# Kernel tuning notes

Measured on AMD Instinct MI355X. Metric: run time of the kernel, lower is better.

Reference implementation:

```python
import jax, jax.numpy as jnp
import numpy as np

T, B, I, H, LBL = 200, 1024, 128, 128, 4


def setup_inputs() -> dict:
    key = jax.random.key(0)
    ks = jax.random.split(key, 14)
    si = 1.0 / np.sqrt(I)
    sh = 1.0 / np.sqrt(H)
    inputs = jax.random.normal(ks[0], (T, B, I), jnp.float32)
    lengths = jnp.maximum(jax.random.randint(ks[1], (B,), 1, T + 1), LBL).astype(jnp.int32)
    return {
        "inputs": inputs,
        "lengths": lengths,
        "Wih_g": jax.random.normal(ks[2], (3 * H, I), jnp.float32) * si,
        "Whh_g": jax.random.normal(ks[3], (3 * H, H), jnp.float32) * sh,
        "bih_g": jax.random.normal(ks[4], (3 * H,), jnp.float32) * sh,
        "bhh_g": jax.random.normal(ks[5], (3 * H,), jnp.float32) * sh,
        "Wih_l": jax.random.normal(ks[6], (3 * H, I), jnp.float32) * si,
        "Whh_l": jax.random.normal(ks[7], (3 * H, H), jnp.float32) * sh,
        "bih_l": jax.random.normal(ks[8], (3 * H,), jnp.float32) * sh,
        "bhh_l": jax.random.normal(ks[9], (3 * H,), jnp.float32) * sh,
        "A1": jax.random.normal(ks[10], (H, H), jnp.float32) * sh,
        "A2": jax.random.normal(ks[11], (H, H), jnp.float32) * sh,
        "v1": jax.random.normal(ks[12], (1, H), jnp.float32) * sh,
        "label_len": LBL,
    }


def gru(x, Wih, Whh, bih, bhh):
    # x: [T, B, I] time-major. PyTorch GRU cell semantics.
    Bq, Hq = x.shape[1], Whh.shape[1]
    gi_all = jnp.einsum('tbi,gi->tbg', x, Wih) + bih  # precompute input projections [T,B,3H]
    def step(h, gi):
        gh = h @ Whh.T + bhh
        ir, iz, inn = jnp.split(gi, 3, axis=-1)
        hr, hz, hn = jnp.split(gh, 3, axis=-1)
        r = jax.nn.sigmoid(ir + hr)
        z = jax.nn.sigmoid(iz + hz)
        n = jnp.tanh(inn + r * hn)
        h = (1.0 - z) * n + z * h
        return h, h
    h0 = jnp.zeros((Bq, Hq), x.dtype)
    _, hs = jax.lax.scan(step, h0, gi_all)
    return hs  # [T, B, H]


def reference(inputs, lengths, Wih_g, Whh_g, bih_g, bhh_g,
              Wih_l, Whh_l, bih_l, bhh_l, A1, A2, v1, label_len):
    h_g = gru(inputs, Wih_g, Whh_g, bih_g, bhh_g)  # [T,B,H]
    h_l = gru(inputs, Wih_l, Whh_l, bih_l, bhh_l)  # [T,B,H]
    # attention score per step s: v1(sigmoid(A1 h_l + A2 h_g)), query-independent
    pre = jax.nn.sigmoid(jnp.einsum('tbh,gh->tbg', h_l, A1) +
                         jnp.einsum('tbh,gh->tbg', h_g, A2))
    scores = jnp.einsum('tbg,og->tbo', pre, v1)  # [T,B,1]
    # per-t output = cumsum_{s<=t}(score*h_l) + h_g[t]
    out = jnp.cumsum(scores * h_l, axis=0) + h_g  # [T,B,H]
    out_b = jnp.transpose(out, (1, 0, 2))  # [B,T,H]
    # gather last label_len timesteps of each sequence: h[b,k] = out[L_b-label_len+k, b]
    idx = lengths[:, None].astype(jnp.int32) - label_len + jnp.arange(label_len, dtype=jnp.int32)[None, :]
    idx = jnp.clip(idx, 0, out_b.shape[1] - 1)  # [B, label_len]
    h = jnp.take_along_axis(out_b, idx[:, :, None], axis=1)  # [B, label_len, H]
    return h
```

## Files before the change

### kernel.cpp

```cpp
#include <hip/hip_runtime.h>
#include <stdint.h>


typedef __attribute__((ext_vector_type(8))) short short8;
typedef __attribute__((ext_vector_type(4))) float float4v;

#define LDS_BARRIER() asm volatile("s_waitcnt lgkmcnt(0)\n\ts_barrier" ::: "memory")

__device__ inline float bf2f(unsigned short u){
  union { unsigned int i; float f; } v; v.i = ((unsigned int)u) << 16; return v.f;
}
__device__ inline unsigned short f2bf(float f){
  union { float f; unsigned int i; } v; v.f = f;
  unsigned int x = v.i;
  return (unsigned short)((x + 0x7fffu + ((x >> 16) & 1u)) >> 16);
}
__device__ inline float sigm(float x){ return __builtin_amdgcn_rcpf(1.0f + __expf(-x)); }

__global__ void k_prep(unsigned short* hl_slot, unsigned short* hg_slot, float* cum,
                       const float* A1, const float* A2, unsigned short* a12)
{
  int i = blockIdx.x * blockDim.x + threadIdx.x;
  hl_slot[i] = 0;
  hg_slot[i] = 0;
  cum[i] = 0.0f;
  if (i < 32768) {
    a12[i] = f2bf((i < 16384) ? A1[i] : A2[i - 16384]);
  }
}

__global__ void k_xcast(const float* __restrict__ x, unsigned short* __restrict__ xb)
{
  int i8 = blockIdx.x * blockDim.x + threadIdx.x;
  int t = i8 >> 14;
  int rem = i8 & 16383;
  int b = rem >> 4, c = rem & 15;
  int m = b & 15, bg = b >> 4;
  const float4* xf = (const float4*)(x + ((size_t)t * 131072 + (size_t)b * 128 + c * 8));
  float4 a = xf[0], bb = xf[1];
  short8 o;
  o[0]=(short)f2bf(a.x); o[1]=(short)f2bf(a.y); o[2]=(short)f2bf(a.z); o[3]=(short)f2bf(a.w);
  o[4]=(short)f2bf(bb.x); o[5]=(short)f2bf(bb.y); o[6]=(short)f2bf(bb.z); o[7]=(short)f2bf(bb.w);
  *(short8*)(xb + (size_t)t * 131072 + (size_t)bg * 2048 + c * 128 + m * 8) = o;
}

__global__ __launch_bounds__(512, 2) void k_scan(
    const unsigned short* __restrict__ xb,
    const float* __restrict__ Wih_g, const float* __restrict__ Whh_g,
    const float* __restrict__ bih_g, const float* __restrict__ bhh_g,
    const float* __restrict__ Wih_l, const float* __restrict__ Whh_l,
    const float* __restrict__ bih_l, const float* __restrict__ bhh_l,
    unsigned short* __restrict__ hl_seq, unsigned short* __restrict__ hg_seq,
    int tc, int t0)
{
  __shared__ __align__(16) unsigned short hb[2][2048];
  int tid = threadIdx.x;
  int w = tid >> 6, L = tid & 63, l15 = L & 15, q = L >> 4;
  int gru = blockIdx.x & 1;
  int bg = blockIdx.x >> 1;
  const float* Wih = gru ? Wih_l : Wih_g;
  const float* Whh = gru ? Whh_l : Whh_g;
  const float* bih = gru ? bih_l : bih_g;
  const float* bhh = gru ? bhh_l : bhh_g;
  unsigned short* myseq = gru ? hl_seq : hg_seq;

  int col = w * 16 + l15;
  int cch = w * 2 + (l15 >> 3);
  int cj  = l15 & 7;

  short8 Wi[3][4], Wh[3][4];
  #pragma unroll
  for (int G = 0; G < 3; G++) {
    int row = G * 128 + col;
    #pragma unroll
    for (int kf = 0; kf < 4; kf++) {
      const float4* p0 = (const float4*)(Wih + (size_t)row * 128 + kf * 32 + q * 8);
      const float4* p1 = (const float4*)(Whh + (size_t)row * 128 + kf * 32 + q * 8);
      float4 a0 = p0[0], a1 = p0[1], b0f = p1[0], b1f = p1[1];
      short8 si, sh;
      si[0]=(short)f2bf(a0.x); si[1]=(short)f2bf(a0.y); si[2]=(short)f2bf(a0.z); si[3]=(short)f2bf(a0.w);
      si[4]=(short)f2bf(a1.x); si[5]=(short)f2bf(a1.y); si[6]=(short)f2bf(a1.z); si[7]=(short)f2bf(a1.w);
      sh[0]=(short)f2bf(b0f.x); sh[1]=(short)f2bf(b0f.y); sh[2]=(short)f2bf(b0f.z); sh[3]=(short)f2bf(b0f.w);
      sh[4]=(short)f2bf(b1f.x); sh[5]=(short)f2bf(b1f.y); sh[6]=(short)f2bf(b1f.z); sh[7]=(short)f2bf(b1f.w);
      Wi[G][kf] = si; Wh[G][kf] = sh;
    }
  }
  float br  = bih[col]       + bhh[col];
  float bz  = bih[128 + col] + bhh[128 + col];
  float bin = bih[256 + col];
  float bnh = bhh[256 + col];

  float hold[4];
  #pragma unroll
  for (int r = 0; r < 4; r++) {
    int m = q * 4 + r;
    unsigned short u = myseq[(size_t)(tc - 1) * 131072 + (size_t)bg * 2048 + cch * 128 + m * 8 + cj];
    hold[r] = bf2f(u);
    hb[0][cch * 128 + m * 8 + cj] = u;
  }

  short8 x2[2][4];
  const unsigned short* xlane = xb + (size_t)bg * 2048 + q * 128 + l15 * 8;
  {
    const unsigned short* px = xlane + (size_t)t0 * 131072;
    #pragma unroll
    for (int kf = 0; kf < 4; kf++) x2[0][kf] = *(const short8*)(px + kf * 512);
    int t1 = t0 + (tc > 1 ? 1 : 0);
    const unsigned short* py = xlane + (size_t)t1 * 131072;
    #pragma unroll
    for (int kf = 0; kf < 4; kf++) x2[1][kf] = *(const short8*)(py + kf * 512);
  }
  __syncthreads();

  unsigned short* opq = myseq + (size_t)bg * 2048 + cch * 128 + q * 32 + cj;
  unsigned int* hbw = (unsigned int*)&hb[0][0];
  int wdw = (2 * w + (l15 >> 3)) * 64 + ((l15 & 6) >> 1);
  bool wlane = (L & 1) == 0;

  auto step = [&](int s, int pin, int pout) {
    short8 Ah[4];
    #pragma unroll
    for (int kf = 0; kf < 4; kf++)
      Ah[kf] = *(const short8*)&hb[pin][(kf * 4 + q) * 128 + l15 * 8];

    float4v rx = (float4v){0.f,0.f,0.f,0.f}, zx = rx, nx = rx;
    #pragma unroll
    for (int kf = 0; kf < 4; kf++) rx = __builtin_amdgcn_mfma_f32_16x16x32_bf16(x2[pin][kf], Wi[0][kf], rx, 0,0,0);
    #pragma unroll
    for (int kf = 0; kf < 4; kf++) zx = __builtin_amdgcn_mfma_f32_16x16x32_bf16(x2[pin][kf], Wi[1][kf], zx, 0,0,0);
    #pragma unroll
    for (int kf = 0; kf < 4; kf++) nx = __builtin_amdgcn_mfma_f32_16x16x32_bf16(x2[pin][kf], Wi[2][kf], nx, 0,0,0);

    {
      int t2 = t0 + (s + 2 < tc ? s + 2 : tc - 1);
      const unsigned short* px = xlane + (size_t)t2 * 131072;
      #pragma unroll
      for (int kf = 0; kf < 4; kf++) x2[pin][kf] = *(const short8*)(px + kf * 512);
    }

    float4v rh = (float4v){0.f,0.f,0.f,0.f}, zh = rh, nh = rh;
    #pragma unroll
    for (int kf = 0; kf < 4; kf++) rh = __builtin_amdgcn_mfma_f32_16x16x32_bf16(Ah[kf], Wh[0][kf], rh, 0,0,0);
    #pragma unroll
    for (int kf = 0; kf < 4; kf++) zh = __builtin_amdgcn_mfma_f32_16x16x32_bf16(Ah[kf], Wh[1][kf], zh, 0,0,0);
    #pragma unroll
    for (int kf = 0; kf < 4; kf++) nh = __builtin_amdgcn_mfma_f32_16x16x32_bf16(Ah[kf], Wh[2][kf], nh, 0,0,0);

    float cr[4], cz[4], cn[4];
    #pragma unroll
    for (int r = 0; r < 4; r++) { cr[r] = rx[r] + br; cz[r] = zx[r] + bz; cn[r] = nx[r] + bin; }

    unsigned int* hbo = hbw + pout * 1024 + wdw;
    #pragma unroll
    for (int r = 0; r < 4; r++) {
      float er = __expf(-(rh[r] + cr[r]));
      float ez = __expf(-(zh[r] + cz[r]));
      float pr = 1.0f + er, pz = 1.0f + ez;
      float inv = __builtin_amdgcn_rcpf(pr * pz);
      float rr = pz * inv;
      float zz = pr * inv;
      float y  = cn[r] + rr * (nh[r] + bnh);
      float em = __expf(-2.0f * y);
      float nn = 2.0f * __builtin_amdgcn_rcpf(1.0f + em) - 1.0f;
      float hn = nn + zz * (hold[r] - nn);
      hold[r] = hn;
      unsigned short hu = f2bf(hn);
      opq[r * 8] = hu;
      unsigned int hv = (unsigned int)hu;
      unsigned int ov = (unsigned int)__shfl_xor((int)hv, 1);
      if (wlane) hbo[(4 * q + r) * 4] = hv | (ov << 16);
    }
    opq += 131072;
    LDS_BARRIER();
  };

  int s = 0;
  for (; s + 1 < tc; s += 2) { step(s, 0, 1); step(s + 1, 1, 0); }
  if (s < tc) step(s, 0, 1);
}

__global__ __launch_bounds__(512) void k_score(const unsigned short* __restrict__ hl_seq,
                                               const unsigned short* __restrict__ hg_seq,
                                               const unsigned short* __restrict__ a12,
                                               const float* __restrict__ v1,
                                               float* __restrict__ score, int tc)
{
  __shared__ __align__(16) unsigned short M1[128][136];
  __shared__ __align__(16) unsigned short M2[128][136];
  int tid = threadIdx.x;
  int w = tid >> 6, L = tid & 63;
  int l15 = L & 15, q = L >> 4;
  int s = blockIdx.x;
  int bghalf = blockIdx.y * 32;

  #pragma unroll
  for (int it = 0; it < 4; it++) {
    int f8 = it * 512 + tid;
    *(short8*)&M1[f8 >> 4][(f8 & 15) * 8] = *(const short8*)(a12 + (size_t)f8 * 8);
    *(short8*)&M2[f8 >> 4][(f8 & 15) * 8] = *(const short8*)(a12 + 16384 + (size_t)f8 * 8);
  }
  __syncthreads();

  float v1v[8];
  #pragma unroll
  for (int nt = 0; nt < 8; nt++) v1v[nt] = v1[nt * 16 + l15];

  short8 Fl[4], Fg[4], Pl[4], Pg[4];
  {
    size_t base = (size_t)s * 131072 + (size_t)(bghalf + w) * 2048 + q * 128 + l15 * 8;
    #pragma unroll
    for (int kf = 0; kf < 4; kf++) {
      Fl[kf] = *(const short8*)(hl_seq + base + kf * 512);
      Fg[kf] = *(const short8*)(hg_seq + base + kf * 512);
    }
  }
  #pragma unroll
  for (int it = 0; it < 4; it++) {
    int bg = bghalf + it * 8 + w;
    if (it + 1 < 4) {
      size_t base = (size_t)s * 131072 + (size_t)(bghalf + (it + 1) * 8 + w) * 2048 + q * 128 + l15 * 8;
      #pragma unroll
      for (int kf = 0; kf < 4; kf++) {
        Pl[kf] = *(const short8*)(hl_seq + base + kf * 512);
        Pg[kf] = *(const short8*)(hg_seq + base + kf * 512);
      }
    }
    float4v acc[8];
    #pragma unroll
    for (int nt = 0; nt < 8; nt++) {
      float4v a = (float4v){0.f, 0.f, 0.f, 0.f};
      #pragma unroll
      for (int kf = 0; kf < 4; kf++)
        a = __builtin_amdgcn_mfma_f32_16x16x32_bf16(
            Fl[kf], *(const short8*)&M1[nt * 16 + l15][kf * 32 + q * 8], a, 0, 0, 0);
      #pragma unroll
      for (int kf = 0; kf < 4; kf++)
        a = __builtin_amdgcn_mfma_f32_16x16x32_bf16(
            Fg[kf], *(const short8*)&M2[nt * 16 + l15][kf * 32 + q * 8], a, 0, 0, 0);
      acc[nt] = a;
    }
    float p4[4];
    #pragma unroll
    for (int r = 0; r < 4; r++) {
      float sum = 0.f;
      #pragma unroll
      for (int nt = 0; nt < 8; nt++) sum += v1v[nt] * sigm(acc[nt][r]);
      sum += __shfl_xor(sum, 1, 16);
      sum += __shfl_xor(sum, 2, 16);
      sum += __shfl_xor(sum, 4, 16);
      sum += __shfl_xor(sum, 8, 16);
      p4[r] = sum;
    }
    if (l15 == 0) {
      #pragma unroll
      for (int r = 0; r < 4; r++)
        score[(size_t)(bg * 16 + q * 4 + r) * tc + s] = p4[r];
    }
    #pragma unroll
    for (int kf = 0; kf < 4; kf++) { Fl[kf] = Pl[kf]; Fg[kf] = Pg[kf]; }
  }
}

__global__ __launch_bounds__(256) void k_cum(const float* __restrict__ score,
                                             const unsigned short* __restrict__ hl_seq,
                                             const unsigned short* __restrict__ hg_seq,
                                             const int* __restrict__ lengths,
                                             float* __restrict__ cum,
                                             float* __restrict__ out, int tc, int t0)
{
  __shared__ __align__(16) unsigned short hlL[100 * 256];
  __shared__ float scL[2][100];
  int tid = threadIdx.x;
  int b2 = tid >> 7, j = tid & 127;
  int b0 = blockIdx.x * 2;
  int b = b0 + b2;
  int base = b2 * 128 + j;
  int bg0 = b0 >> 4, m0 = b0 & 15;

  float c = cum[(size_t)b * 128 + j];
  int cap0 = lengths[b] - 4;

  float hgv[4];
  #pragma unroll
  for (int d = 0; d < 4; d++) {
    int sl = cap0 + d - t0;
    hgv[d] = (sl >= 0 && sl < tc)
      ? bf2f(hg_seq[(size_t)sl * 131072 + (size_t)(b >> 4) * 2048 + (j >> 3) * 128 + (b & 15) * 8 + (j & 7)])
      : 0.f;
  }

  for (int seg = 0; seg < tc; seg += 100) {
    int len = (tc - seg < 100) ? (tc - seg) : 100;
    __syncthreads();
    for (int f8 = tid; f8 < len * 32; f8 += 256) {
      int sl = f8 >> 5, r8 = f8 & 31;
      int bb = r8 >> 4, ch = r8 & 15;
      *(short8*)&hlL[(size_t)f8 * 8] =
          *(const short8*)(hl_seq + (size_t)(seg + sl) * 131072 + (size_t)bg0 * 2048
                           + ch * 128 + (m0 + bb) * 8);
    }
    for (int i = tid; i < 2 * len; i += 256) {
      int bb = (i >= len) ? 1 : 0;
      int sl = i - bb * len;
      scL[bb][sl] = score[(size_t)(b0 + bb) * tc + seg + sl];
    }
    __syncthreads();

    int sl = 0;
    for (; sl + 5 <= len; sl += 5) {
      float h[5], sc[5];
      #pragma unroll
      for (int k = 0; k < 5; k++) {
        h[k] = bf2f(hlL[(size_t)(sl + k) * 256 + base]);
        sc[k] = scL[b2][sl + k];
      }
      #pragma unroll
      for (int k = 0; k < 5; k++) {
        c += sc[k] * h[k];
        int d = (t0 + seg + sl + k) - cap0;
        if ((unsigned)d < 4u)
          out[((size_t)b * 4 + d) * 128 + j] = c + hgv[d];
      }
    }
    for (; sl < len; sl++) {
      c += scL[b2][sl] * bf2f(hlL[(size_t)sl * 256 + base]);
      int d = (t0 + seg + sl) - cap0;
      if ((unsigned)d < 4u)
        out[((size_t)b * 4 + d) * 128 + j] = c + hgv[d];
    }
  }
  cum[(size_t)b * 128 + j] = c;
}

extern "C" void kernel_launch(void* const* d_in, const int* in_sizes, int n_in,
                              void* d_out, int out_size, void* d_ws, size_t ws_size,
                              hipStream_t stream)
{
  const float* x     = (const float*)d_in[0];
  const int* lengths = (const int*)d_in[1];
  const float* Wih_g = (const float*)d_in[2];
  const float* Whh_g = (const float*)d_in[3];
  const float* bih_g = (const float*)d_in[4];
  const float* bhh_g = (const float*)d_in[5];
  const float* Wih_l = (const float*)d_in[6];
  const float* Whh_l = (const float*)d_in[7];
  const float* bih_l = (const float*)d_in[8];
  const float* bhh_l = (const float*)d_in[9];
  const float* A1    = (const float*)d_in[10];
  const float* A2    = (const float*)d_in[11];
  const float* v1    = (const float*)d_in[12];
  float* out = (float*)d_out;

  const size_t XB = (size_t)200 * 1024 * 128 * 2;
  const size_t fixed = 65536 + 524288 + XB;
  const int cands[8] = {200, 100, 50, 25, 10, 5, 2, 1};
  int tc = 0;
  for (int i = 0; i < 8; i++) {
    int T = cands[i];
    size_t need = 2 * (size_t)T * 1024 * 128 * 2
                + (size_t)T * 1024 * 4
                + fixed;
    if (need <= ws_size) { tc = T; break; }
  }
  if (!tc) return;

  char* wsb = (char*)d_ws;
  size_t o = 0;
  unsigned short* a12 = (unsigned short*)(wsb + o); o += 65536;
  float* cum   = (float*)(wsb + o); o += 524288;
  unsigned short* xb = (unsigned short*)(wsb + o); o += XB;
  unsigned short* hl  = (unsigned short*)(wsb + o); o += (size_t)tc * 1024 * 128 * 2;
  unsigned short* hg  = (unsigned short*)(wsb + o); o += (size_t)tc * 1024 * 128 * 2;
  float* score = (float*)(wsb + o);

  unsigned short* hl_slot = hl + (size_t)(tc - 1) * 1024 * 128;
  unsigned short* hg_slot = hg + (size_t)(tc - 1) * 1024 * 128;

  k_prep<<<512, 256, 0, stream>>>(hl_slot, hg_slot, cum, A1, A2, a12);
  k_xcast<<<12800, 256, 0, stream>>>(x, xb);
  int nch = 200 / tc;
  for (int c = 0; c < nch; c++) {
    k_scan<<<128, 512, 0, stream>>>(xb, Wih_g, Whh_g, bih_g, bhh_g,
                                    Wih_l, Whh_l, bih_l, bhh_l, hl, hg, tc, c * tc);
    k_score<<<dim3(tc, 2), 512, 0, stream>>>(hl, hg, a12, v1, score, tc);
    k_cum<<<512, 256, 0, stream>>>(score, hl, hg, lengths, cum, out, tc, c * tc);
  }
}
```

Baseline: 444.0 us.

## Overlap GRU scan with previous chunk's epilogue and next chunk's cast in one kernel

Merges the recurrent scan, the score/cumsum epilogue and the input bf16 cast into a single combined kernel per time chunk. Blocks 0-127 run the scan for chunk c, blocks 128-191 run the fused score and cumsum epilogue for chunk c-1, and the remaining blocks cast the inputs for chunk c+1. Hidden-state buffers are double-buffered so the chunks can proceed concurrently. The aim is to hide epilogue and cast work behind the latency-bound scan and to cut launches from three per chunk to one. The cost is more launches overall with smaller chunks (cap 50), a larger LDS footprint in the combined kernel that may reduce occupancy, and an extra epilogue launch at the end.

```diff
diff --git a/kernel.cpp b/kernel.cpp
--- a/kernel.cpp
+++ b/kernel.cpp
@@ -17,52 +17,24 @@
 }
 __device__ inline float sigm(float x){ return __builtin_amdgcn_rcpf(1.0f + __expf(-x)); }
 
-__global__ void k_prep(unsigned short* hl_slot, unsigned short* hg_slot, float* cum,
-                       const float* A1, const float* A2, unsigned short* a12)
-{
-  int i = blockIdx.x * blockDim.x + threadIdx.x;
-  hl_slot[i] = 0;
-  hg_slot[i] = 0;
-  cum[i] = 0.0f;
-  if (i < 32768) {
-    a12[i] = f2bf((i < 16384) ? A1[i] : A2[i - 16384]);
-  }
-}
-
-__global__ void k_xcast(const float* __restrict__ x, unsigned short* __restrict__ xb)
-{
-  int i8 = blockIdx.x * blockDim.x + threadIdx.x;
-  int t = i8 >> 14;
-  int rem = i8 & 16383;
-  int b = rem >> 4, c = rem & 15;
-  int m = b & 15, bg = b >> 4;
-  const float4* xf = (const float4*)(x + ((size_t)t * 131072 + (size_t)b * 128 + c * 8));
-  float4 a = xf[0], bb = xf[1];
-  short8 o;
-  o[0]=(short)f2bf(a.x); o[1]=(short)f2bf(a.y); o[2]=(short)f2bf(a.z); o[3]=(short)f2bf(a.w);
-  o[4]=(short)f2bf(bb.x); o[5]=(short)f2bf(bb.y); o[6]=(short)f2bf(bb.z); o[7]=(short)f2bf(bb.w);
-  *(short8*)(xb + (size_t)t * 131072 + (size_t)bg * 2048 + c * 128 + m * 8) = o;
-}
-
-__global__ __launch_bounds__(512, 2) void k_scan(
+__device__ __forceinline__ void scan_body(
+    unsigned short* hb,
     const unsigned short* __restrict__ xb,
     const float* __restrict__ Wih_g, const float* __restrict__ Whh_g,
     const float* __restrict__ bih_g, const float* __restrict__ bhh_g,
     const float* __restrict__ Wih_l, const float* __restrict__ Whh_l,
     const float* __restrict__ bih_l, const float* __restrict__ bhh_l,
-    unsigned short* __restrict__ hl_seq, unsigned short* __restrict__ hg_seq,
-    int tc, int t0)
-{
-  __shared__ __align__(16) unsigned short hb[2][2048];
-  int tid = threadIdx.x;
+    unsigned short* __restrict__ wrseq,
+    const unsigned short* __restrict__ prevseq,
+    int tc, int t0, int bid, int tid)
+{
   int w = tid >> 6, L = tid & 63, l15 = L & 15, q = L >> 4;
-  int gru = blockIdx.x & 1;
-  int bg = blockIdx.x >> 1;
+  int gru = bid & 1;
+  int bg = bid >> 1;
   const float* Wih = gru ? Wih_l : Wih_g;
   const float* Whh = gru ? Whh_l : Whh_g;
   const float* bih = gru ? bih_l : bih_g;
   const float* bhh = gru ? bhh_l : bhh_g;
-  unsigned short* myseq = gru ? hl_seq : hg_seq;
 
   int col = w * 16 + l15;
   int cch = w * 2 + (l15 >> 3);
@@ -94,9 +66,9 @@
   #pragma unroll
   for (int r = 0; r < 4; r++) {
     int m = q * 4 + r;
-    unsigned short u = myseq[(size_t)(tc - 1) * 131072 + (size_t)bg * 2048 + cch * 128 + m * 8 + cj];
+    unsigned short u = prevseq[(size_t)(tc - 1) * 131072 + (size_t)bg * 2048 + cch * 128 + m * 8 + cj];
     hold[r] = bf2f(u);
-    hb[0][cch * 128 + m * 8 + cj] = u;
+    hb[cch * 128 + m * 8 + cj] = u;
   }
 
   short8 x2[2][4];
@@ -112,8 +84,8 @@
   }
   __syncthreads();
 
-  unsigned short* opq = myseq + (size_t)bg * 2048 + cch * 128 + q * 32 + cj;
-  unsigned int* hbw = (unsigned int*)&hb[0][0];
+  unsigned short* opq = wrseq + (size_t)bg * 2048 + cch * 128 + q * 32 + cj;
+  unsigned int* hbw = (unsigned int*)hb;
   int wdw = (2 * w + (l15 >> 3)) * 64 + ((l15 & 6) >> 1);
   bool wlane = (L & 1) == 0;
 
@@ -121,7 +93,15 @@
     short8 Ah[4];
     #pragma unroll
     for (int kf = 0; kf < 4; kf++)
-      Ah[kf] = *(const short8*)&hb[pin][(kf * 4 + q) * 128 + l15 * 8];
+      Ah[kf] = *(const short8*)&hb[pin * 2048 + (kf * 4 + q) * 128 + l15 * 8];
+
+    float4v rh = (float4v){0.f,0.f,0.f,0.f}, zh = rh, nh = rh;
+    #pragma unroll
+    for (int kf = 0; kf < 4; kf++) rh = __builtin_amdgcn_mfma_f32_16x16x32_bf16(Ah[kf], Wh[0][kf], rh, 0,0,0);
+    #pragma unroll
+    for (int kf = 0; kf < 4; kf++) zh = __builtin_amdgcn_mfma_f32_16x16x32_bf16(Ah[kf], Wh[1][kf], zh, 0,0,0);
+    #pragma unroll
+    for (int kf = 0; kf < 4; kf++) nh = __builtin_amdgcn_mfma_f32_16x16x32_bf16(Ah[kf], Wh[2][kf], nh, 0,0,0);
 
     float4v rx = (float4v){0.f,0.f,0.f,0.f}, zx = rx, nx = rx;
     #pragma unroll
@@ -138,28 +118,16 @@
       for (int kf = 0; kf < 4; kf++) x2[pin][kf] = *(const short8*)(px + kf * 512);
     }
 
-    float4v rh = (float4v){0.f,0.f,0.f,0.f}, zh = rh, nh = rh;
-    #pragma unroll
-    for (int kf = 0; kf < 4; kf++) rh = __builtin_amdgcn_mfma_f32_16x16x32_bf16(Ah[kf], Wh[0][kf], rh, 0,0,0);
-    #pragma unroll
-    for (int kf = 0; kf < 4; kf++) zh = __builtin_amdgcn_mfma_f32_16x16x32_bf16(Ah[kf], Wh[1][kf], zh, 0,0,0);
-    #pragma unroll
-    for (int kf = 0; kf < 4; kf++) nh = __builtin_amdgcn_mfma_f32_16x16x32_bf16(Ah[kf], Wh[2][kf], nh, 0,0,0);
-
-    float cr[4], cz[4], cn[4];
-    #pragma unroll
-    for (int r = 0; r < 4; r++) { cr[r] = rx[r] + br; cz[r] = zx[r] + bz; cn[r] = nx[r] + bin; }
-
     unsigned int* hbo = hbw + pout * 1024 + wdw;
     #pragma unroll
     for (int r = 0; r < 4; r++) {
-      float er = __expf(-(rh[r] + cr[r]));
-      float ez = __expf(-(zh[r] + cz[r]));
+      float er = __expf(-(rh[r] + rx[r] + br));
+      float ez = __expf(-(zh[r] + zx[r] + bz));
       float pr = 1.0f + er, pz = 1.0f + ez;
       float inv = __builtin_amdgcn_rcpf(pr * pz);
       float rr = pz * inv;
       float zz = pr * inv;
-      float y  = cn[r] + rr * (nh[r] + bnh);
+      float y  = nx[r] + bin + rr * (nh[r] + bnh);
       float em = __expf(-2.0f * y);
       float nn = 2.0f * __builtin_amdgcn_rcpf(1.0f + em) - 1.0f;
       float hn = nn + zz * (hold[r] - nn);
@@ -179,157 +147,192 @@
   if (s < tc) step(s, 0, 1);
 }
 
-__global__ __launch_bounds__(512) void k_score(const unsigned short* __restrict__ hl_seq,
-                                               const unsigned short* __restrict__ hg_seq,
-                                               const unsigned short* __restrict__ a12,
-                                               const float* __restrict__ v1,
-                                               float* __restrict__ score, int tc)
-{
-  __shared__ __align__(16) unsigned short M1[128][136];
-  __shared__ __align__(16) unsigned short M2[128][136];
-  int tid = threadIdx.x;
-  int w = tid >> 6, L = tid & 63;
-  int l15 = L & 15, q = L >> 4;
-  int s = blockIdx.x;
-  int bghalf = blockIdx.y * 32;
-
-  #pragma unroll
-  for (int it = 0; it < 4; it++) {
-    int f8 = it * 512 + tid;
-    *(short8*)&M1[f8 >> 4][(f8 & 15) * 8] = *(const short8*)(a12 + (size_t)f8 * 8);
-    *(short8*)&M2[f8 >> 4][(f8 & 15) * 8] = *(const short8*)(a12 + 16384 + (size_t)f8 * 8);
-  }
-  __syncthreads();
-
-  float v1v[8];
-  #pragma unroll
-  for (int nt = 0; nt < 8; nt++) v1v[nt] = v1[nt * 16 + l15];
-
-  short8 Fl[4], Fg[4], Pl[4], Pg[4];
-  {
-    size_t base = (size_t)s * 131072 + (size_t)(bghalf + w) * 2048 + q * 128 + l15 * 8;
+__device__ __forceinline__ void epilogue_body(
+    unsigned short* hlL, float* scF4,
+    const unsigned short* __restrict__ hl_rd,
+    const unsigned short* __restrict__ hg_rd,
+    const unsigned short* __restrict__ a12,
+    const float* __restrict__ v1,
+    const int* __restrict__ lengths,
+    float* __restrict__ cum, float* __restrict__ out,
+    int e, int tc, int bg, int tid)
+{
+  int w = tid >> 6, L = tid & 63, l15 = L & 15, q = L >> 4;
+  int ch = w & 3;
+  int tst = w >> 2;
+
+  short8 B1[2][4], B2[2][4];
+  float v1v[2];
+  #pragma unroll
+  for (int ntl = 0; ntl < 2; ntl++) {
+    int g = (2 * ch + ntl) * 16 + l15;
     #pragma unroll
     for (int kf = 0; kf < 4; kf++) {
-      Fl[kf] = *(const short8*)(hl_seq + base + kf * 512);
-      Fg[kf] = *(const short8*)(hg_seq + base + kf * 512);
-    }
-  }
-  #pragma unroll
-  for (int it = 0; it < 4; it++) {
-    int bg = bghalf + it * 8 + w;
-    if (it + 1 < 4) {
-      size_t base = (size_t)s * 131072 + (size_t)(bghalf + (it + 1) * 8 + w) * 2048 + q * 128 + l15 * 8;
-      #pragma unroll
-      for (int kf = 0; kf < 4; kf++) {
-        Pl[kf] = *(const short8*)(hl_seq + base + kf * 512);
-        Pg[kf] = *(const short8*)(hg_seq + base + kf * 512);
-      }
-    }
-    float4v acc[8];
-    #pragma unroll
-    for (int nt = 0; nt < 8; nt++) {
+      B1[ntl][kf] = *(const short8*)(a12 + (size_t)g * 128 + kf * 32 + q * 8);
+      B2[ntl][kf] = *(const short8*)(a12 + 16384 + (size_t)g * 128 + kf * 32 + q * 8);
+    }
+    v1v[ntl] = v1[g];
+  }
+
+  for (int t = tst; t < tc; t += 2) {
+    size_t base = (size_t)t * 131072 + (size_t)bg * 2048 + q * 128 + l15 * 8;
+    short8 Fl[4], Fg[4];
+    #pragma unroll
+    for (int kf = 0; kf < 4; kf++) {
+      Fl[kf] = *(const short8*)(hl_rd + base + kf * 512);
+      Fg[kf] = *(const short8*)(hg_rd + base + kf * 512);
+    }
+    float4v acc[2];
+    #pragma unroll
+    for (int ntl = 0; ntl < 2; ntl++) {
       float4v a = (float4v){0.f, 0.f, 0.f, 0.f};
       #pragma unroll
       for (int kf = 0; kf < 4; kf++)
-        a = __builtin_amdgcn_mfma_f32_16x16x32_bf16(
-            Fl[kf], *(const short8*)&M1[nt * 16 + l15][kf * 32 + q * 8], a, 0, 0, 0);
+        a = __builtin_amdgcn_mfma_f32_16x16x32_bf16(Fl[kf], B1[ntl][kf], a, 0, 0, 0);
       #pragma unroll
       for (int kf = 0; kf < 4; kf++)
-        a = __builtin_amdgcn_mfma_f32_16x16x32_bf16(
-            Fg[kf], *(const short8*)&M2[nt * 16 + l15][kf * 32 + q * 8], a, 0, 0, 0);
-      acc[nt] = a;
-    }
-    float p4[4];
+        a = __builtin_amdgcn_mfma_f32_16x16x32_bf16(Fg[kf], B2[ntl][kf], a, 0, 0, 0);
+      acc[ntl] = a;
+    }
     #pragma unroll
     for (int r = 0; r < 4; r++) {
-      float sum = 0.f;
+      float s = v1v[0] * sigm(acc[0][r]) + v1v[1] * sigm(acc[1][r]);
+      s += __shfl_xor(s, 1, 16);
+      s += __shfl_xor(s, 2, 16);
+      s += __shfl_xor(s, 4, 16);
+      s += __shfl_xor(s, 8, 16);
+      if (l15 == 0) scF4[ch * 800 + t * 16 + q * 4 + r] = s;
+    }
+  }
+  __syncthreads();
+  for (int i = tid; i < tc * 16; i += 512)
+    scF4[i] = scF4[i] + scF4[800 + i] + scF4[1600 + i] + scF4[2400 + i];
+
+  float cacc[4]; int capv[4], bl4[4], j4[4], bidx[4];
+  #pragma unroll
+  for (int k = 0; k < 4; k++) {
+    int pi = tid + k * 512;
+    int bl = pi & 15, j = (pi >> 4) & 127;
+    bl4[k] = bl; j4[k] = j;
+    int b = bg * 16 + bl; bidx[k] = b;
+    cacc[k] = cum[(size_t)b * 128 + j];
+    capv[k] = lengths[b] - 4;
+  }
+  int t0g = e * tc;
+  for (int seg = 0; seg < tc; seg += 10) {
+    int len = (tc - seg < 10) ? (tc - seg) : 10;
+    __syncthreads();
+    for (int f8 = tid; f8 < len * 256; f8 += 512) {
+      int tt = f8 >> 8, idx = f8 & 255;
+      *(short8*)&hlL[tt * 2048 + idx * 8] =
+          *(const short8*)(hl_rd + (size_t)(seg + tt) * 131072 + (size_t)bg * 2048 + idx * 8);
+    }
+    __syncthreads();
+    for (int tt = 0; tt < len; tt++) {
+      int t = seg + tt;
       #pragma unroll
-      for (int nt = 0; nt < 8; nt++) sum += v1v[nt] * sigm(acc[nt][r]);
-      sum += __shfl_xor(sum, 1, 16);
-      sum += __shfl_xor(sum, 2, 16);
-      sum += __shfl_xor(sum, 4, 16);
-      sum += __shfl_xor(sum, 8, 16);
-      p4[r] = sum;
-    }
-    if (l15 == 0) {
-      #pragma unroll
-      for (int r = 0; r < 4; r++)
-        score[(size_t)(bg * 16 + q * 4 + r) * tc + s] = p4[r];
-    }
-    #pragma unroll
-    for (int kf = 0; kf < 4; kf++) { Fl[kf] = Pl[kf]; Fg[kf] = Pg[kf]; }
-  }
-}
-
-__global__ __launch_bounds__(256) void k_cum(const float* __restrict__ score,
-                                             const unsigned short* __restrict__ hl_seq,
-                                             const unsigned short* __restrict__ hg_seq,
-                                             const int* __restrict__ lengths,
-                                             float* __restrict__ cum,
-                                             float* __restrict__ out, int tc, int t0)
-{
-  __shared__ __align__(16) unsigned short hlL[100 * 256];
-  __shared__ float scL[2][100];
-  int tid = threadIdx.x;
-  int b2 = tid >> 7, j = tid & 127;
-  int b0 = blockIdx.x * 2;
-  int b = b0 + b2;
-  int base = b2 * 128 + j;
-  int bg0 = b0 >> 4, m0 = b0 & 15;
-
-  float c = cum[(size_t)b * 128 + j];
-  int cap0 = lengths[b] - 4;
-
-  float hgv[4];
-  #pragma unroll
-  for (int d = 0; d < 4; d++) {
-    int sl = cap0 + d - t0;
-    hgv[d] = (sl >= 0 && sl < tc)
-      ? bf2f(hg_seq[(size_t)sl * 131072 + (size_t)(b >> 4) * 2048 + (j >> 3) * 128 + (b & 15) * 8 + (j & 7)])
-      : 0.f;
-  }
-
-  for (int seg = 0; seg < tc; seg += 100) {
-    int len = (tc - seg < 100) ? (tc - seg) : 100;
-    __syncthreads();
-    for (int f8 = tid; f8 < len * 32; f8 += 256) {
-      int sl = f8 >> 5, r8 = f8 & 31;
-      int bb = r8 >> 4, ch = r8 & 15;
-      *(short8*)&hlL[(size_t)f8 * 8] =
-          *(const short8*)(hl_seq + (size_t)(seg + sl) * 131072 + (size_t)bg0 * 2048
-                           + ch * 128 + (m0 + bb) * 8);
-    }
-    for (int i = tid; i < 2 * len; i += 256) {
-      int bb = (i >= len) ? 1 : 0;
-      int sl = i - bb * len;
-      scL[bb][sl] = score[(size_t)(b0 + bb) * tc + seg + sl];
-    }
-    __syncthreads();
-
-    int sl = 0;
-    for (; sl + 5 <= len; sl += 5) {
-      float h[5], sc[5];
-      #pragma unroll
-      for (int k = 0; k < 5; k++) {
-        h[k] = bf2f(hlL[(size_t)(sl + k) * 256 + base]);
-        sc[k] = scL[b2][sl + k];
+      for (int k = 0; k < 4; k++) {
+        int fj = (j4[k] >> 3) * 128 + bl4[k] * 8 + (j4[k] & 7);
+        float h = bf2f(hlL[tt * 2048 + fj]);
+        cacc[k] += scF4[t * 16 + bl4[k]] * h;
+        int d = (t0g + t) - capv[k];
+        if ((unsigned)d < 4u) {
+          float hgv = bf2f(hg_rd[(size_t)t * 131072 + (size_t)bg * 2048 + fj]);
+          out[((size_t)bidx[k] * 4 + d) * 128 + j4[k]] = cacc[k] + hgv;
+        }
       }
-      #pragma unroll
-      for (int k = 0; k < 5; k++) {
-        c += sc[k] * h[k];
-        int d = (t0 + seg + sl + k) - cap0;
-        if ((unsigned)d < 4u)
-          out[((size_t)b * 4 + d) * 128 + j] = c + hgv[d];
-      }
-    }
-    for (; sl < len; sl++) {
-      c += scL[b2][sl] * bf2f(hlL[(size_t)sl * 256 + base]);
-      int d = (t0 + seg + sl) - cap0;
-      if ((unsigned)d < 4u)
-        out[((size_t)b * 4 + d) * 128 + j] = c + hgv[d];
-    }
-  }
-  cum[(size_t)b * 128 + j] = c;
+    }
+  }
+  #pragma unroll
+  for (int k = 0; k < 4; k++)
+    cum[(size_t)bidx[k] * 128 + j4[k]] = cacc[k];
+}
+
+__global__ __launch_bounds__(512) void k_pre(const float* __restrict__ x,
+                                             unsigned short* __restrict__ xb,
+                                             unsigned short* hl_slot1, unsigned short* hg_slot1,
+                                             float* cum,
+                                             const float* A1, const float* A2,
+                                             unsigned short* a12, int tc)
+{
+  int i = blockIdx.x * 512 + threadIdx.x;
+  hl_slot1[i] = 0;
+  hg_slot1[i] = 0;
+  cum[i] = 0.0f;
+  if (i < 32768) a12[i] = f2bf((i < 16384) ? A1[i] : A2[i - 16384]);
+  int items = tc * 16384;
+  for (int i8 = i; i8 < items; i8 += 131072) {
+    int t = i8 >> 14, rem = i8 & 16383, b = rem >> 4, chn = rem & 15;
+    const float4* xf = (const float4*)(x + (size_t)t * 131072 + (size_t)b * 128 + chn * 8);
+    float4 a = xf[0], bb = xf[1];
+    short8 o;
+    o[0]=(short)f2bf(a.x); o[1]=(short)f2bf(a.y); o[2]=(short)f2bf(a.z); o[3]=(short)f2bf(a.w);
+    o[4]=(short)f2bf(bb.x); o[5]=(short)f2bf(bb.y); o[6]=(short)f2bf(bb.z); o[7]=(short)f2bf(bb.w);
+    *(short8*)(xb + (size_t)t * 131072 + (size_t)(b >> 4) * 2048 + chn * 128 + (b & 15) * 8) = o;
+  }
+}
+
+__global__ __launch_bounds__(512, 2) void k_combo(
+    const float* __restrict__ x, unsigned short* __restrict__ xb,
+    const float* __restrict__ Wih_g, const float* __restrict__ Whh_g,
+    const float* __restrict__ bih_g, const float* __restrict__ bhh_g,
+    const float* __restrict__ Wih_l, const float* __restrict__ Whh_l,
+    const float* __restrict__ bih_l, const float* __restrict__ bhh_l,
+    const unsigned short* __restrict__ a12, const float* __restrict__ v1,
+    const int* __restrict__ lengths, float* __restrict__ cum, float* __restrict__ out,
+    unsigned short* hlA, unsigned short* hgA,
+    unsigned short* hlB, unsigned short* hgB,
+    int c, int tc, int nch)
+{
+  __shared__ __align__(16) unsigned short hb[2 * 2048];
+  __shared__ __align__(16) unsigned short hlL[10 * 2048];
+  __shared__ float scF4[4 * 800];
+  int bid = blockIdx.x, tid = threadIdx.x;
+
+  if (bid < 128) {
+    int p = c & 1;
+    unsigned short* hl_wr = p ? hlB : hlA;
+    unsigned short* hg_wr = p ? hgB : hgA;
+    const unsigned short* hl_pv = p ? hlA : hlB;
+    const unsigned short* hg_pv = p ? hgA : hgB;
+    int gru = bid & 1;
+    scan_body(hb, xb, Wih_g, Whh_g, bih_g, bhh_g, Wih_l, Whh_l, bih_l, bhh_l,
+              gru ? hl_wr : hg_wr, gru ? hl_pv : hg_pv, tc, c * tc, bid, tid);
+  } else if (bid < 192) {
+    if (c == 0) return;
+    int e = c - 1, pe = e & 1;
+    epilogue_body(hlL, scF4, pe ? hlB : hlA, pe ? hgB : hgA, a12, v1,
+                  lengths, cum, out, e, tc, bid - 128, tid);
+  } else {
+    int cx = c + 1;
+    if (cx >= nch) return;
+    int gtid = (bid - 192) * 512 + tid;
+    int items = tc * 16384;
+    for (int i8 = gtid; i8 < items; i8 += 32768) {
+      int tl = i8 >> 14, rem = i8 & 16383, b = rem >> 4, chn = rem & 15;
+      int t = cx * tc + tl;
+      const float4* xf = (const float4*)(x + (size_t)t * 131072 + (size_t)b * 128 + chn * 8);
+      float4 a = xf[0], bb = xf[1];
+      short8 o;
+      o[0]=(short)f2bf(a.x); o[1]=(short)f2bf(a.y); o[2]=(short)f2bf(a.z); o[3]=(short)f2bf(a.w);
+      o[4]=(short)f2bf(bb.x); o[5]=(short)f2bf(bb.y); o[6]=(short)f2bf(bb.z); o[7]=(short)f2bf(bb.w);
+      *(short8*)(xb + (size_t)t * 131072 + (size_t)(b >> 4) * 2048 + chn * 128 + (b & 15) * 8) = o;
+    }
+  }
+}
+
+__global__ __launch_bounds__(512, 2) void k_epi(
+    const unsigned short* __restrict__ a12, const float* __restrict__ v1,
+    const int* __restrict__ lengths, float* __restrict__ cum, float* __restrict__ out,
+    unsigned short* hlA, unsigned short* hgA,
+    unsigned short* hlB, unsigned short* hgB,
+    int e, int tc)
+{
+  __shared__ __align__(16) unsigned short hlL[10 * 2048];
+  __shared__ float scF4[4 * 800];
+  int pe = e & 1;
+  epilogue_body(hlL, scF4, pe ? hlB : hlA, pe ? hgB : hgA, a12, v1,
+                lengths, cum, out, e, tc, blockIdx.x, threadIdx.x);
 }
 
 extern "C" void kernel_launch(void* const* d_in, const int* in_sizes, int n_in,
@@ -353,36 +356,37 @@
 
   const size_t XB = (size_t)200 * 1024 * 128 * 2;
   const size_t fixed = 65536 + 524288 + XB;
-  const int cands[8] = {200, 100, 50, 25, 10, 5, 2, 1};
+  const int cands[6] = {50, 25, 10, 5, 2, 1};
   int tc = 0;
-  for (int i = 0; i < 8; i++) {
+  for (int i = 0; i < 6; i++) {
     int T = cands[i];
-    size_t need = 2 * (size_t)T * 1024 * 128 * 2
-                + (size_t)T * 1024 * 4
-                + fixed;
-    if (need <= ws_size) { tc = T; break; }
+    size_t CH = (size_t)T * 1024 * 128 * 2;
+    if (fixed + 4 * CH <= ws_size) { tc = T; break; }
   }
   if (!tc) return;
+  size_t CH = (size_t)tc * 1024 * 128 * 2;
 
   char* wsb = (char*)d_ws;
   size_t o = 0;
   unsigned short* a12 = (unsigned short*)(wsb + o); o += 65536;
-  float* cum   = (float*)(wsb + o); o += 524288;
-  unsigned short* xb = (unsigned short*)(wsb + o); o += XB;
-  unsigned short* hl  = (unsigned short*)(wsb + o); o += (size_t)tc * 1024 * 128 * 2;
-  unsigned short* hg  = (unsigned short*)(wsb + o); o += (size_t)tc * 1024 * 128 * 2;
-  float* score = (float*)(wsb + o);
-
-  unsigned short* hl_slot = hl + (size_t)(tc - 1) * 1024 * 128;
-  unsigned short* hg_slot = hg + (size_t)(tc - 1) * 1024 * 128;
-
-  k_prep<<<512, 256, 0, stream>>>(hl_slot, hg_slot, cum, A1, A2, a12);
-  k_xcast<<<12800, 256, 0, stream>>>(x, xb);
+  float* cum          = (float*)(wsb + o);          o += 524288;
+  unsigned short* xb  = (unsigned short*)(wsb + o); o += XB;
+  unsigned short* hlA = (unsigned short*)(wsb + o); o += CH;
+  unsigned short* hgA = (unsigned short*)(wsb + o); o += CH;
+  unsigned short* hlB = (unsigned short*)(wsb + o); o += CH;
+  unsigned short* hgB = (unsigned short*)(wsb + o); o += CH;
+
+  unsigned short* hl_slot1 = hlB + (size_t)(tc - 1) * 131072;
+  unsigned short* hg_slot1 = hgB + (size_t)(tc - 1) * 131072;
+
   int nch = 200 / tc;
+  k_pre<<<256, 512, 0, stream>>>(x, xb, hl_slot1, hg_slot1, cum, A1, A2, a12, tc);
   for (int c = 0; c < nch; c++) {
-    k_scan<<<128, 512, 0, stream>>>(xb, Wih_g, Whh_g, bih_g, bhh_g,
-                                    Wih_l, Whh_l, bih_l, bhh_l, hl, hg, tc, c * tc);
-    k_score<<<dim3(tc, 2), 512, 0, stream>>>(hl, hg, a12, v1, score, tc);
-    k_cum<<<512, 256, 0, stream>>>(score, hl, hg, lengths, cum, out, tc, c * tc);
-  }
-}
+    k_combo<<<256, 512, 0, stream>>>(x, xb, Wih_g, Whh_g, bih_g, bhh_g,
+                                     Wih_l, Whh_l, bih_l, bhh_l,
+                                     a12, v1, lengths, cum, out,
+                                     hlA, hgA, hlB, hgB, c, tc, nch);
+  }
+  k_epi<<<64, 512, 0, stream>>>(a12, v1, lengths, cum, out,
+                                hlA, hgA, hlB, hgB, nch - 1, tc);
+}
```

After: 562.4 us. 1.27x slower.
